# Kernel optimization log

Hardware: AMD Instinct MI355X
Metric: run time of the kernel (lower is better)

## Reference

```python
import jax, jax.numpy as jnp
import numpy as np

B, N, IN_DIM = 8, 4096, 768
H, DH = 12, 64
D_MODEL = H * DH
SCALE = DH ** -0.5


def setup_inputs() -> dict:
    key = jax.random.key(0)
    k1, k2, k3 = jax.random.split(key, 3)
    x = jax.random.normal(k1, (B, N, IN_DIM), dtype=jnp.float32)
    w_qkv = jax.random.normal(k2, (3 * D_MODEL, IN_DIM), dtype=jnp.float32) * 0.02
    w_lin = jax.random.normal(k3, (IN_DIM, D_MODEL), dtype=jnp.float32) * 0.02
    b_lin = jnp.zeros((IN_DIM,), dtype=jnp.float32)
    return {"x": x, "w_qkv": w_qkv, "w_lin": w_lin, "b_lin": b_lin}


def reference(x, w_qkv, w_lin, b_lin):
    # qkv projection: [B, N, 3*d_model]
    qkv = jnp.einsum('bni,oi->bno', x, w_qkv)
    # unflatten to heads, move head dim forward: [B, H, N, 3*dh]
    qkv = qkv.reshape(B, N, H, 3 * DH).transpose(0, 2, 1, 3)
    q, k, v = jnp.split(qkv, 3, axis=-1)  # each [B, H, N, dh]
    q = jax.nn.softmax(q, axis=-1) * SCALE   # softmax over feature dim
    k = jax.nn.softmax(k, axis=-2)           # softmax over token dim N
    # context: [B, H, dh, dh]
    context = jnp.einsum('bhnd,bhne->bhde', k, v)
    # output per head: [B, H, N, dh]
    o = jnp.einsum('bhnd,bhde->bhne', q, context)
    # merge heads: [B, N, d_model]
    o = o.transpose(0, 2, 1, 3).reshape(B, N, D_MODEL)
    return jnp.einsum('bnd,od->bno', o, w_lin) + b_lin
```

## Files before the change

### kernel.cpp

```cpp
#include <hip/hip_runtime.h>
#include <hip/hip_bf16.h>

#define BATCH 8
#define NTOK 4096
#define IN_DIM 768
#define NHEAD 12
#define DH 64
#define D_MODEL 768
#define OC 2304
#define SCALE 0.125f

typedef _Float16 f16x8 __attribute__((ext_vector_type(8)));
typedef float f32x4 __attribute__((ext_vector_type(4)));

union HalfPack { uint4 u; f16x8 h; };

__device__ __forceinline__ void stage_payload(const float* __restrict__ src,
                                              char* lds_hi, char* lds_lo, int off)
{
    float4 v0 = *(const float4*)(src);
    float4 v1 = *(const float4*)(src + 4);
    float f[8] = {v0.x, v0.y, v0.z, v0.w, v1.x, v1.y, v1.z, v1.w};
    HalfPack hi, lo;
#pragma unroll
    for (int e = 0; e < 8; ++e) {
        _Float16 h = (_Float16)f[e];
        hi.h[e] = h;
        lo.h[e] = (_Float16)(f[e] - (float)h);
    }
    *(uint4*)(lds_hi + off) = hi.u;
    *(uint4*)(lds_lo + off) = lo.u;
}

template<bool BIAS>
__global__ __launch_bounds__(256, 2)
void gemm_nt_mfma(const float* __restrict__ A, const float* __restrict__ W,
                  const float* __restrict__ bias, float* __restrict__ C,
                  int M, int K, int Nout)
{
    __shared__ f16x8 Ah[512], Al[512], Wh[512], Wl[512];
    const int tid  = threadIdx.x;
    const int lane = tid & 63;
    const int wave = tid >> 6;
    const int wm = wave >> 1, wn = wave & 1;
    const int bm = blockIdx.y * 128, bn = blockIdx.x * 128;

    f32x4 acc[4][4] = {};

    for (int k0 = 0; k0 < K; k0 += 32) {
#pragma unroll
        for (int pi = 0; pi < 2; ++pi) {
            int p = tid + pi * 256;
            int l = p & 63, f = p >> 6;
            int row = f * 16 + (l & 15);
            int ko  = 8 * (l >> 4);
            stage_payload(A + (size_t)(bm + row) * K + k0 + ko, (char*)Ah, (char*)Al, p * 16);
            stage_payload(W + (size_t)(bn + row) * K + k0 + ko, (char*)Wh, (char*)Wl, p * 16);
        }
        __syncthreads();

        f16x8 a_h[4], a_l[4], w_h[4], w_l[4];
#pragma unroll
        for (int i = 0; i < 4; ++i) {
            a_h[i] = Ah[(wm * 4 + i) * 64 + lane];
            a_l[i] = Al[(wm * 4 + i) * 64 + lane];
            w_h[i] = Wh[(wn * 4 + i) * 64 + lane];
            w_l[i] = Wl[(wn * 4 + i) * 64 + lane];
        }

#pragma unroll
        for (int i = 0; i < 4; ++i)
#pragma unroll
            for (int j = 0; j < 4; ++j) {
                acc[i][j] = __builtin_amdgcn_mfma_f32_16x16x32_f16(a_h[i], w_h[j], acc[i][j], 0, 0, 0);
                acc[i][j] = __builtin_amdgcn_mfma_f32_16x16x32_f16(a_h[i], w_l[j], acc[i][j], 0, 0, 0);
                acc[i][j] = __builtin_amdgcn_mfma_f32_16x16x32_f16(a_l[i], w_h[j], acc[i][j], 0, 0, 0);
            }
        __syncthreads();
    }

    const int r4 = (lane >> 4) * 4;
    const int cc = lane & 15;
#pragma unroll
    for (int i = 0; i < 4; ++i) {
        int grow = bm + (wm * 4 + i) * 16 + r4;
#pragma unroll
        for (int j = 0; j < 4; ++j) {
            int gcol = bn + (wn * 4 + j) * 16 + cc;
            float badd = BIAS ? bias[gcol] : 0.f;
#pragma unroll
            for (int r = 0; r < 4; ++r)
                C[(size_t)(grow + r) * Nout + gcol] = acc[i][j][r] + badd;
        }
    }
}

#define NCH 16
__global__ __launch_bounds__(256)
void context_kernel(const float* __restrict__ qkv_b, float* __restrict__ ctx,
                    float* __restrict__ colsum)
{
    const int h = blockIdx.x;
    const int n0 = blockIdx.y * (NTOK / NCH);
    const int t = threadIdx.x;
    const int d = t & 63, eb = t >> 6;
    const float* kb = qkv_b + h * 192 + 64;
    const float* vb = kb + 64;
    __shared__ float Ks[16][64];
    __shared__ float Vs[16][64];

    float acc[16];
#pragma unroll
    for (int j = 0; j < 16; ++j) acc[j] = 0.f;
    float psum = 0.f;

    const int r = t >> 4, c4 = t & 15;
    for (int nc = 0; nc < NTOK / NCH; nc += 16) {
        const size_t off = (size_t)(n0 + nc + r) * OC + c4 * 4;
        *(float4*)&Ks[r][c4 * 4] = *(const float4*)(kb + off);
        *(float4*)&Vs[r][c4 * 4] = *(const float4*)(vb + off);
        __syncthreads();
#pragma unroll
        for (int nn = 0; nn < 16; ++nn) {
            float p = __expf(Ks[nn][d]);
            psum += p;
#pragma unroll
            for (int j = 0; j < 16; ++j)
                acc[j] = fmaf(p, Vs[nn][eb * 16 + j], acc[j]);
        }
        __syncthreads();
    }
    float* cp = ctx + ((size_t)h * 64 + d) * 64 + eb * 16;
#pragma unroll
    for (int j = 0; j < 16; ++j) atomicAdd(cp + j, acc[j]);
    if (eb == 0) atomicAdd(colsum + h * 64 + d, psum);
}

__global__ __launch_bounds__(256)
void qsoftmax_kernel(const float* __restrict__ qkv_b, float* __restrict__ qs)
{
    const size_t row = blockIdx.x;
    const int t = threadIdx.x;
    const int hq = t >> 6;
    const int d = t & 63;
    const float* qrow = qkv_b + row * OC;
    float* orow = qs + row * D_MODEL;
#pragma unroll
    for (int hg = 0; hg < NHEAD; hg += 4) {
        int h = hg + hq;
        float v = qrow[h * 192 + d];
        float m = v;
#pragma unroll
        for (int off = 32; off >= 1; off >>= 1) m = fmaxf(m, __shfl_xor(m, off));
        float e = __expf(v - m);
        float s = e;
#pragma unroll
        for (int off = 32; off >= 1; off >>= 1) s += __shfl_xor(s, off);
        orow[h * 64 + d] = e / s * SCALE;
    }
}

__global__ __launch_bounds__(256)
void mt_kernel(const float* __restrict__ ctx, const float* __restrict__ colsum,
               const float* __restrict__ wlin, float* __restrict__ MT)
{
    const int h = blockIdx.x;
    const int o0 = blockIdx.y * 64;
    const int t = threadIdx.x;
    const int d = t & 63, og = t >> 6;
    __shared__ float cs[64][65];
    __shared__ float wl[64][65];
    __shared__ float inv_s[64];
    if (t < 64) inv_s[t] = 1.f / colsum[h * 64 + t];
    __syncthreads();
    for (int i = t; i < 4096; i += 256)
        cs[i >> 6][i & 63] = ctx[(size_t)h * 4096 + i] * inv_s[i >> 6];
#pragma unroll
    for (int j = 0; j < 4; ++j) {
        int idx = t + j * 256;
        int r = idx >> 4, c4 = idx & 15;
        float4 v = *(const float4*)(wlin + (size_t)(o0 + r) * D_MODEL + h * 64 + c4 * 4);
        wl[r][c4 * 4 + 0] = v.x; wl[r][c4 * 4 + 1] = v.y;
        wl[r][c4 * 4 + 2] = v.z; wl[r][c4 * 4 + 3] = v.w;
    }
    __syncthreads();
#pragma unroll
    for (int oo = 0; oo < 16; ++oo) {
        int o = og * 16 + oo;
        float s = 0.f;
#pragma unroll
        for (int e = 0; e < 64; ++e)
            s = fmaf(wl[o][e], cs[d][e], s);
        MT[(size_t)(o0 + o) * D_MODEL + h * 64 + d] = s;
    }
}

extern "C" void kernel_launch(void* const* d_in, const int* in_sizes, int n_in,
                              void* d_out, int out_size, void* d_ws, size_t ws_size,
                              hipStream_t stream)
{
    const float* x     = (const float*)d_in[0];
    const float* w_qkv = (const float*)d_in[1];
    const float* w_lin = (const float*)d_in[2];
    const float* b_lin = (const float*)d_in[3];
    float* out = (float*)d_out;

    float* ws      = (float*)d_ws;
    float* qkv_b   = ws;
    float* qs_b    = qkv_b + (size_t)NTOK * OC;
    float* MT_b    = qs_b + (size_t)NTOK * D_MODEL;
    float* ctx_all = MT_b + (size_t)D_MODEL * D_MODEL;
    float* sum_all = ctx_all + (size_t)BATCH * NHEAD * DH * DH;

    hipMemsetAsync(ctx_all, 0,
                   ((size_t)BATCH * NHEAD * DH * DH + BATCH * D_MODEL) * sizeof(float),
                   stream);

    for (int b = 0; b < BATCH; ++b) {
        const float* x_b = x + (size_t)b * NTOK * IN_DIM;
        float* ctx_b = ctx_all + (size_t)b * NHEAD * DH * DH;
        float* sum_b = sum_all + (size_t)b * D_MODEL;
        float* out_b = out + (size_t)b * NTOK * D_MODEL;

        dim3 g1(OC / 128, NTOK / 128);
        gemm_nt_mfma<false><<<g1, 256, 0, stream>>>(x_b, w_qkv, nullptr, qkv_b,
                                                    NTOK, IN_DIM, OC);

        dim3 g2(NHEAD, NCH);
        context_kernel<<<g2, 256, 0, stream>>>(qkv_b, ctx_b, sum_b);

        qsoftmax_kernel<<<NTOK, 256, 0, stream>>>(qkv_b, qs_b);

        dim3 g4(NHEAD, D_MODEL / 64);
        mt_kernel<<<g4, 256, 0, stream>>>(ctx_b, sum_b, w_lin, MT_b);

        dim3 g5(D_MODEL / 128, NTOK / 128);
        gemm_nt_mfma<true><<<g5, 256, 0, stream>>>(qs_b, MT_b, b_lin, out_b,
                                                   NTOK, D_MODEL, D_MODEL);
    }
}
```

Before: 1.939 ms.

## Pre-split GEMM operands into fp16 hi/lo buffers and load via global_load_lds

Moves the fp32-to-fp16 hi/lo split out of the GEMM inner loop into a separate split kernel for x and w_qkv. The producer kernels (q softmax, M^T) now write the hi/lo halves directly. The GEMM then stages tiles with direct global-to-LDS 16-byte loads and raises occupancy to 3 blocks per CU. This removes per-tile conversion ALU work and VGPR round-trips from the GEMM. The cost is extra global traffic: x is written and re-read as two fp16 arrays per batch, plus extra kernel launches.

```diff
diff --git a/kernel.cpp b/kernel.cpp
--- a/kernel.cpp
+++ b/kernel.cpp
@@ -11,32 +11,43 @@
 #define SCALE 0.125f
 
 typedef _Float16 f16x8 __attribute__((ext_vector_type(8)));
+typedef _Float16 f16x4 __attribute__((ext_vector_type(4)));
 typedef float f32x4 __attribute__((ext_vector_type(4)));
 
-union HalfPack { uint4 u; f16x8 h; };
-
-__device__ __forceinline__ void stage_payload(const float* __restrict__ src,
-                                              char* lds_hi, char* lds_lo, int off)
-{
-    float4 v0 = *(const float4*)(src);
-    float4 v1 = *(const float4*)(src + 4);
-    float f[8] = {v0.x, v0.y, v0.z, v0.w, v1.x, v1.y, v1.z, v1.w};
-    HalfPack hi, lo;
-#pragma unroll
-    for (int e = 0; e < 8; ++e) {
-        _Float16 h = (_Float16)f[e];
-        hi.h[e] = h;
-        lo.h[e] = (_Float16)(f[e] - (float)h);
-    }
-    *(uint4*)(lds_hi + off) = hi.u;
-    *(uint4*)(lds_lo + off) = lo.u;
+__device__ __forceinline__ void gload16(const void* g, void* l)
+{
+    __builtin_amdgcn_global_load_lds(
+        (const __attribute__((address_space(1))) void*)g,
+        (__attribute__((address_space(3))) void*)l, 16, 0, 0);
+}
+
+__global__ __launch_bounds__(256)
+void split_f32_kernel(const float* __restrict__ in, _Float16* __restrict__ hi,
+                      _Float16* __restrict__ lo, int n4)
+{
+    int i = blockIdx.x * 256 + threadIdx.x;
+    const int stride = gridDim.x * 256;
+    for (; i < n4; i += stride) {
+        float4 v = ((const float4*)in)[i];
+        float f[4] = {v.x, v.y, v.z, v.w};
+        f16x4 h, l;
+#pragma unroll
+        for (int e = 0; e < 4; ++e) {
+            _Float16 hh = (_Float16)f[e];
+            h[e] = hh;
+            l[e] = (_Float16)(f[e] - (float)hh);
+        }
+        ((f16x4*)hi)[i] = h;
+        ((f16x4*)lo)[i] = l;
+    }
 }
 
 template<bool BIAS>
-__global__ __launch_bounds__(256, 2)
-void gemm_nt_mfma(const float* __restrict__ A, const float* __restrict__ W,
-                  const float* __restrict__ bias, float* __restrict__ C,
-                  int M, int K, int Nout)
+__global__ __launch_bounds__(256, 3)
+void gemm_nt_f16pair(const _Float16* __restrict__ Ahg, const _Float16* __restrict__ Alg,
+                     const _Float16* __restrict__ Whg, const _Float16* __restrict__ Wlg,
+                     const float* __restrict__ bias, float* __restrict__ C,
+                     int M, int K, int Nout)
 {
     __shared__ f16x8 Ah[512], Al[512], Wh[512], Wl[512];
     const int tid  = threadIdx.x;
@@ -45,18 +56,24 @@
     const int wm = wave >> 1, wn = wave & 1;
     const int bm = blockIdx.y * 128, bn = blockIdx.x * 128;
 
+    const int r0 = wave * 16 + (lane & 15);
+    const int ko = 8 * (lane >> 4);
+    const size_t aoff0 = (size_t)(bm + r0) * K + ko;
+    const size_t aoff1 = aoff0 + (size_t)64 * K;
+    const size_t woff0 = (size_t)(bn + r0) * K + ko;
+    const size_t woff1 = woff0 + (size_t)64 * K;
+
     f32x4 acc[4][4] = {};
 
     for (int k0 = 0; k0 < K; k0 += 32) {
-#pragma unroll
-        for (int pi = 0; pi < 2; ++pi) {
-            int p = tid + pi * 256;
-            int l = p & 63, f = p >> 6;
-            int row = f * 16 + (l & 15);
-            int ko  = 8 * (l >> 4);
-            stage_payload(A + (size_t)(bm + row) * K + k0 + ko, (char*)Ah, (char*)Al, p * 16);
-            stage_payload(W + (size_t)(bn + row) * K + k0 + ko, (char*)Wh, (char*)Wl, p * 16);
-        }
+        gload16(Ahg + aoff0 + k0, &Ah[wave * 64]);
+        gload16(Ahg + aoff1 + k0, &Ah[wave * 64 + 256]);
+        gload16(Alg + aoff0 + k0, &Al[wave * 64]);
+        gload16(Alg + aoff1 + k0, &Al[wave * 64 + 256]);
+        gload16(Whg + woff0 + k0, &Wh[wave * 64]);
+        gload16(Whg + woff1 + k0, &Wh[wave * 64 + 256]);
+        gload16(Wlg + woff0 + k0, &Wl[wave * 64]);
+        gload16(Wlg + woff1 + k0, &Wl[wave * 64 + 256]);
         __syncthreads();
 
         f16x8 a_h[4], a_l[4], w_h[4], w_l[4];
@@ -137,14 +154,14 @@
 }
 
 __global__ __launch_bounds__(256)
-void qsoftmax_kernel(const float* __restrict__ qkv_b, float* __restrict__ qs)
+void qsoftmax_kernel(const float* __restrict__ qkv_b,
+                     _Float16* __restrict__ qsh, _Float16* __restrict__ qsl)
 {
     const size_t row = blockIdx.x;
     const int t = threadIdx.x;
     const int hq = t >> 6;
     const int d = t & 63;
     const float* qrow = qkv_b + row * OC;
-    float* orow = qs + row * D_MODEL;
 #pragma unroll
     for (int hg = 0; hg < NHEAD; hg += 4) {
         int h = hg + hq;
@@ -156,13 +173,18 @@
         float s = e;
 #pragma unroll
         for (int off = 32; off >= 1; off >>= 1) s += __shfl_xor(s, off);
-        orow[h * 64 + d] = e / s * SCALE;
+        float val = e / s * SCALE;
+        _Float16 hh = (_Float16)val;
+        size_t idx = row * D_MODEL + h * 64 + d;
+        qsh[idx] = hh;
+        qsl[idx] = (_Float16)(val - (float)hh);
     }
 }
 
 __global__ __launch_bounds__(256)
 void mt_kernel(const float* __restrict__ ctx, const float* __restrict__ colsum,
-               const float* __restrict__ wlin, float* __restrict__ MT)
+               const float* __restrict__ wlin,
+               _Float16* __restrict__ MTh, _Float16* __restrict__ MTl)
 {
     const int h = blockIdx.x;
     const int o0 = blockIdx.y * 64;
@@ -191,7 +213,10 @@
 #pragma unroll
         for (int e = 0; e < 64; ++e)
             s = fmaf(wl[o][e], cs[d][e], s);
-        MT[(size_t)(o0 + o) * D_MODEL + h * 64 + d] = s;
+        _Float16 hh = (_Float16)s;
+        size_t idx = (size_t)(o0 + o) * D_MODEL + h * 64 + d;
+        MTh[idx] = hh;
+        MTl[idx] = (_Float16)(s - (float)hh);
     }
 }
 
@@ -207,14 +232,23 @@
 
     float* ws      = (float*)d_ws;
     float* qkv_b   = ws;
-    float* qs_b    = qkv_b + (size_t)NTOK * OC;
-    float* MT_b    = qs_b + (size_t)NTOK * D_MODEL;
-    float* ctx_all = MT_b + (size_t)D_MODEL * D_MODEL;
+    float* ctx_all = qkv_b + (size_t)NTOK * OC;
     float* sum_all = ctx_all + (size_t)BATCH * NHEAD * DH * DH;
+    _Float16* wqh  = (_Float16*)(sum_all + (size_t)BATCH * D_MODEL);
+    _Float16* wql  = wqh + (size_t)OC * IN_DIM;
+    _Float16* xh   = wql + (size_t)OC * IN_DIM;
+    _Float16* xl   = xh + (size_t)NTOK * IN_DIM;
+    _Float16* MTh  = xl + (size_t)NTOK * IN_DIM;
+    _Float16* MTl  = MTh + (size_t)D_MODEL * D_MODEL;
+    _Float16* qsh = xh;
+    _Float16* qsl = xl;
 
     hipMemsetAsync(ctx_all, 0,
                    ((size_t)BATCH * NHEAD * DH * DH + BATCH * D_MODEL) * sizeof(float),
                    stream);
+
+    split_f32_kernel<<<(OC * IN_DIM / 4 + 255) / 256, 256, 0, stream>>>(
+        w_qkv, wqh, wql, OC * IN_DIM / 4);
 
     for (int b = 0; b < BATCH; ++b) {
         const float* x_b = x + (size_t)b * NTOK * IN_DIM;
@@ -222,20 +256,22 @@
         float* sum_b = sum_all + (size_t)b * D_MODEL;
         float* out_b = out + (size_t)b * NTOK * D_MODEL;
 
+        split_f32_kernel<<<2048, 256, 0, stream>>>(x_b, xh, xl, NTOK * IN_DIM / 4);
+
         dim3 g1(OC / 128, NTOK / 128);
-        gemm_nt_mfma<false><<<g1, 256, 0, stream>>>(x_b, w_qkv, nullptr, qkv_b,
-                                                    NTOK, IN_DIM, OC);
+        gemm_nt_f16pair<false><<<g1, 256, 0, stream>>>(xh, xl, wqh, wql, nullptr,
+                                                       qkv_b, NTOK, IN_DIM, OC);
 
         dim3 g2(NHEAD, NCH);
         context_kernel<<<g2, 256, 0, stream>>>(qkv_b, ctx_b, sum_b);
 
-        qsoftmax_kernel<<<NTOK, 256, 0, stream>>>(qkv_b, qs_b);
+        qsoftmax_kernel<<<NTOK, 256, 0, stream>>>(qkv_b, qsh, qsl);
 
         dim3 g4(NHEAD, D_MODEL / 64);
-        mt_kernel<<<g4, 256, 0, stream>>>(ctx_b, sum_b, w_lin, MT_b);
+        mt_kernel<<<g4, 256, 0, stream>>>(ctx_b, sum_b, w_lin, MTh, MTl);
 
         dim3 g5(D_MODEL / 128, NTOK / 128);
-        gemm_nt_mfma<true><<<g5, 256, 0, stream>>>(qs_b, MT_b, b_lin, out_b,
-                                                   NTOK, D_MODEL, D_MODEL);
-    }
-}
+        gemm_nt_f16pair<true><<<g5, 256, 0, stream>>>(qsh, qsl, MTh, MTl, b_lin,
+                                                      out_b, NTOK, D_MODEL, D_MODEL);
+    }
+}
```

Result: slower. 1.978 ms (+2.0%).
